# Optimization experiments

Hardware: AMD Instinct MI355X
Metric: run time of the kernel (lower is better)

Reference implementation:

```python
import jax, jax.numpy as jnp
import numpy as np
from jax import lax

HID = 256
FLAT = 32 * 9 * 9  # ShallowConv on 84x84: (84-8)/4+1=20 -> (20-4)/2+1=9 ; 32 ch


def _conv(x, w, b, stride):
    y = lax.conv_general_dilated(x, w, window_strides=(stride, stride),
                                 padding='VALID',
                                 dimension_numbers=('NCHW', 'OIHW', 'NCHW'))
    return y + b[None, :, None, None]


def setup_inputs() -> dict:
    key = jax.random.key(0)
    ks = jax.random.split(key, 20)
    seq, batch, c, h, w = 80, 128, 4, 84, 84
    n_out = 18
    f32 = jnp.float32
    inp = {}
    inp['obs'] = jax.random.uniform(ks[0], (seq, batch, c, h, w), dtype=f32)
    inp['mask'] = (jax.random.uniform(ks[1], (seq, batch)) > 0.05).astype(f32)
    inp['lstm_h'] = jax.random.normal(ks[2], (1, batch, HID), dtype=f32)
    inp['lstm_c'] = jax.random.normal(ks[3], (1, batch, HID), dtype=f32)
    inp['behaviour_actions'] = jax.random.randint(ks[4], (seq, batch), 0, n_out)
    def init(k, shape, fan_in):
        return (jax.random.normal(k, shape, dtype=f32) / np.sqrt(fan_in)).astype(f32)
    inp['conv1_w'] = init(ks[5], (16, c, 8, 8), c * 64)
    inp['conv1_b'] = jnp.zeros((16,), f32)
    inp['conv2_w'] = init(ks[6], (32, 16, 4, 4), 16 * 16)
    inp['conv2_b'] = jnp.zeros((32,), f32)
    inp['fc_w'] = init(ks[7], (HID, FLAT), FLAT)
    inp['fc_b'] = jnp.zeros((HID,), f32)
    inp['w_ih'] = init(ks[8], (4 * HID, HID), HID)
    inp['w_hh'] = init(ks[9], (4 * HID, HID), HID)
    inp['b_ih'] = jnp.zeros((4 * HID,), f32)
    inp['b_hh'] = jnp.zeros((4 * HID,), f32)
    inp['value_w'] = init(ks[10], (1, HID), HID)
    inp['value_b'] = jnp.zeros((1,), f32)
    inp['logits_w'] = init(ks[11], (n_out, HID), HID)
    inp['logits_b'] = jnp.zeros((n_out,), f32)
    return inp


def reference(obs, mask, lstm_h, lstm_c, behaviour_actions,
              conv1_w, conv1_b, conv2_w, conv2_b, fc_w, fc_b,
              w_ih, w_hh, b_ih, b_hh, value_w, value_b, logits_w, logits_b):
    seq, batch, c, h, w = obs.shape
    x = obs.reshape(seq * batch, c, h, w)
    # body: ShallowConv -> Flatten -> ReLU -> fc -> ReLU
    x = jax.nn.relu(_conv(x, conv1_w, conv1_b, 4))
    x = jax.nn.relu(_conv(x, conv2_w, conv2_b, 2))
    x = x.reshape(seq * batch, FLAT)
    x = jax.nn.relu(x @ fc_w.T + fc_b)
    x = x.reshape(seq, batch, HID)

    def step(carry, xs_t):
        hprev, cprev = carry
        xt, mt = xs_t
        gates = xt @ w_ih.T + b_ih + hprev @ w_hh.T + b_hh  # (batch, 4H)
        i, f, g, o = jnp.split(gates, 4, axis=-1)  # torch gate order i,f,g,o
        i, f, o = jax.nn.sigmoid(i), jax.nn.sigmoid(f), jax.nn.sigmoid(o)
        cn = f * cprev + i * jnp.tanh(g)
        hn = o * jnp.tanh(cn)
        m = mt[:, None]
        return (hn * m, cn * m), hn  # emit pre-mask output, mask states

    (hf, cf), hs = lax.scan(step, (lstm_h[0], lstm_c[0]), (x, mask))
    flat = hs.reshape(seq * batch, HID)
    target_value = flat @ value_w.T + value_b  # (S*B, 1)
    logits = flat @ logits_w.T + logits_b      # (S*B, n_out)
    logp = jax.nn.log_softmax(logits, axis=-1)
    acts = behaviour_actions.reshape(seq * batch)
    target_log_probs = jnp.take_along_axis(logp, acts[:, None], axis=1)
    target_entropy = -jnp.sum(jnp.exp(logp) * logp, axis=-1, keepdims=True)
    return (target_log_probs.reshape(seq, batch, 1),
            target_entropy.reshape(seq, batch, 1),
            target_value.reshape(seq, batch, 1))
```

## Files before the change

### kernel.cpp

```cpp
#include <hip/hip_runtime.h>

typedef unsigned short u16;
typedef unsigned int   u32;
typedef unsigned long long u64;
typedef short    s8v  __attribute__((ext_vector_type(8)));
typedef float    f4v  __attribute__((ext_vector_type(4)));
typedef u64      ul2v __attribute__((ext_vector_type(2)));
typedef _Float16 h2v  __attribute__((ext_vector_type(2)));

#define DEV __device__ __forceinline__

DEV u16 f2bf(float f) {
  u32 u = __builtin_bit_cast(u32, f);
  return (u16)((u + 0x8000u) >> 16);
}
DEV float bf2f(u16 b) { u32 u = ((u32)b) << 16; return __builtin_bit_cast(float, u); }
DEV void splitbf(float f, u16& hi, u16& lo) {
  hi = f2bf(f);
  lo = f2bf(f - bf2f(hi));
}
DEV u16 f2h(float f) {
  _Float16 h = (_Float16)f;
  return __builtin_bit_cast(u16, h);
}
DEV float h2f(u16 b) { _Float16 h = __builtin_bit_cast(_Float16, b); return (float)h; }
DEV float fdot2u(u32 a, u32 b, float c) {
#if __has_builtin(__builtin_amdgcn_fdot2)
  return __builtin_amdgcn_fdot2(__builtin_bit_cast(h2v, a),
                                __builtin_bit_cast(h2v, b), c, false);
#else
  h2v x = __builtin_bit_cast(h2v, a), y = __builtin_bit_cast(h2v, b);
  return c + (float)x[0]*(float)y[0] + (float)x[1]*(float)y[1];
#endif
}
DEV float sigm(float x) { return 1.f / (1.f + __expf(-x)); }
DEV f4v mfma16(s8v a, s8v b, f4v c) {
  return __builtin_amdgcn_mfma_f32_16x16x32_bf16(a, b, c, 0, 0, 0);
}
DEV u32 permpack(u32 a, u32 b) {
#if __has_builtin(__builtin_amdgcn_perm)
  return __builtin_amdgcn_perm(a, b, 0x07060302u);
#else
  return (b >> 16) | (a & 0xffff0000u);
#endif
}
DEV void split8(const float* __restrict__ ap, s8v& Ah, s8v& Al) {
  const float4 v0 = *(const float4*)ap;
  const float4 v1 = *(const float4*)(ap + 4);
  const float f[8] = {v0.x, v0.y, v0.z, v0.w, v1.x, v1.y, v1.z, v1.w};
  uint4 hh, ll;
  u32 hp[4], lp[4];
  #pragma unroll
  for (int i = 0; i < 4; ++i) {
    const u32 ua = __builtin_bit_cast(u32, f[2 * i]);
    const u32 ub = __builtin_bit_cast(u32, f[2 * i + 1]);
    const u32 ta = ua + 0x8000u, tb = ub + 0x8000u;
    hp[i] = permpack(tb, ta);
    const float la = f[2 * i]     - __builtin_bit_cast(float, ta & 0xffff0000u);
    const float lb = f[2 * i + 1] - __builtin_bit_cast(float, tb & 0xffff0000u);
    lp[i] = permpack(__builtin_bit_cast(u32, lb) + 0x8000u,
                     __builtin_bit_cast(u32, la) + 0x8000u);
  }
  hh.x = hp[0]; hh.y = hp[1]; hh.z = hp[2]; hh.w = hp[3];
  ll.x = lp[0]; ll.y = lp[1]; ll.z = lp[2]; ll.w = lp[3];
  Ah = __builtin_bit_cast(s8v, hh);
  Al = __builtin_bit_cast(s8v, ll);
}

__global__ void prep_k(const float* __restrict__ w1, const float* __restrict__ w2,
                       const float* __restrict__ fcw, const float* __restrict__ wih,
                       const float* __restrict__ whh, const float* __restrict__ bih,
                       const float* __restrict__ bhh,
                       u16* __restrict__ w1h, u16* __restrict__ w1l,
                       u16* __restrict__ w2h, u16* __restrict__ w2l,
                       u16* __restrict__ fh,  u16* __restrict__ fl,
                       u16* __restrict__ ih,  u16* __restrict__ il,
                       u16* __restrict__ whhh, float* __restrict__ bsum) {
  const int i0 = blockIdx.x * 256 + threadIdx.x;
  const int st = gridDim.x * 256;
  for (int i = i0; i < 663552; i += st) splitbf(fcw[i], fh[i], fl[i]);
  for (int i = i0; i < 262144; i += st) splitbf(wih[i], ih[i], il[i]);
  for (int i = i0; i < 262144; i += st) whhh[i] = f2h(whh[i]);
  for (int i = i0; i < 4096;   i += st) splitbf(w1[i], w1h[i], w1l[i]);
  for (int i = i0; i < 8192;   i += st) {
    const int oc = i >> 8, k = i & 255;
    const int ky = k >> 6, kx = (k >> 4) & 3, cc = k & 15;
    splitbf(w2[((oc * 16 + cc) * 4 + ky) * 4 + kx], w2h[i], w2l[i]);
  }
  for (int i = i0; i < 1024; i += st) bsum[i] = bih[i] + bhh[i];
}

__global__ __launch_bounds__(256) void conv_k(const float* __restrict__ obs,
    const u16* __restrict__ w1h, const u16* __restrict__ w1l, const float* __restrict__ b1,
    const u16* __restrict__ w2h, const u16* __restrict__ w2l, const float* __restrict__ b2,
    u16* __restrict__ out2h, u16* __restrict__ out2l) {
  __shared__ __align__(16) u16 t1h[6400], t1l[6400];
  const int tid = threadIdx.x, lane = tid & 63, wid = tid >> 6;
  const int l15 = lane & 15, kc = lane >> 4;
  const int n = blockIdx.x;
  s8v bw1h[8], bw1l[8];
  #pragma unroll
  for (int k0 = 0; k0 < 8; ++k0) {
    const int o1 = l15 * 256 + k0 * 32 + kc * 8;
    bw1h[k0] = *(const s8v*)(w1h + o1);
    bw1l[k0] = *(const s8v*)(w1l + o1);
  }
  const float bias1 = b1[l15];
  const float* img = obs + (u64)n * 28224;
  for (int ch = wid; ch < 25; ch += 4) {
    const int p = ch * 16 + l15;
    const int oy = p / 20, ox = p - oy * 20;
    const float* ab = img + oy * 336 + ox * 4;
    f4v ahh = {0,0,0,0}, ahl = {0,0,0,0}, alh = {0,0,0,0};
    #pragma unroll
    for (int k0 = 0; k0 < 8; ++k0) {
      const int kb = k0 * 32 + kc * 8;
      const int c = kb >> 6, ky = (kb >> 3) & 7;
      s8v Ah, Al;
      split8(ab + c * 7056 + ky * 84, Ah, Al);
      ahh = mfma16(Ah, bw1h[k0], ahh);
      ahl = mfma16(Ah, bw1l[k0], ahl);
      alh = mfma16(Al, bw1h[k0], alh);
    }
    const int pr0 = ch * 16 + kc * 4;
    #pragma unroll
    for (int r = 0; r < 4; ++r) {
      float v = fmaxf(ahh[r] + ahl[r] + alh[r] + bias1, 0.f);
      u16 hi, lo; splitbf(v, hi, lo);
      t1h[(pr0 + r) * 16 + l15] = hi;
      t1l[(pr0 + r) * 16 + l15] = lo;
    }
  }
  __syncthreads();
  const float bb2a = b2[l15], bb2b = b2[16 + l15];
  for (int u = wid; u < 12; u += 4) {
    const int ch = u >> 1, ot = u & 1;
    const int p = ch * 16 + l15;
    const int pc = p < 81 ? p : 80;
    const int oy = pc / 9, ox = pc - oy * 9;
    const int base = (oy * 40 + ox * 2) * 16;
    f4v a0 = {0,0,0,0}, a1 = {0,0,0,0}, a2 = {0,0,0,0};
    #pragma unroll
    for (int k0 = 0; k0 < 8; ++k0) {
      const int kb = k0 * 32 + kc * 8;
      const int ky = kb >> 6, kx = (kb >> 4) & 3, c0 = kb & 15;
      const int off = base + (ky * 20 + kx) * 16 + c0;
      s8v Ah = *(const s8v*)(t1h + off);
      s8v Al = *(const s8v*)(t1l + off);
      const int wo = (ot * 16 + l15) * 256 + k0 * 32 + kc * 8;
      s8v Bh = *(const s8v*)(w2h + wo);
      s8v Bl = *(const s8v*)(w2l + wo);
      a0 = mfma16(Ah, Bh, a0);
      a1 = mfma16(Ah, Bl, a1);
      a2 = mfma16(Al, Bh, a2);
    }
    const float bb = ot ? bb2b : bb2a;
    const int oc = ot * 16 + l15;
    u16* dh = out2h + (u64)n * 2592 + oc * 81;
    u16* dl = out2l + (u64)n * 2592 + oc * 81;
    const int pr0 = ch * 16 + kc * 4;
    #pragma unroll
    for (int r = 0; r < 4; ++r) {
      const int pp = pr0 + r;
      if (pp < 81) {
        float v = fmaxf(a0[r] + a1[r] + a2[r] + bb, 0.f);
        u16 hi, lo; splitbf(v, hi, lo);
        dh[pp] = hi;
        dl[pp] = lo;
      }
    }
  }
}

template <int RELU, int OSPLIT>
__global__ __launch_bounds__(256) void gemm3_k(const u16* __restrict__ Ah,
    const u16* __restrict__ Al, const u16* __restrict__ Bh, const u16* __restrict__ Bl,
    const float* __restrict__ bias, void* __restrict__ o1, void* __restrict__ o2,
    int M, int N, int K) {
  __shared__ __align__(16) u16 lAh[4096], lAl[4096];
  __shared__ __align__(16) u16 lBh[4096], lBl[4096];
  const int tid = threadIdx.x, lane = tid & 63, wid = tid >> 6;
  const int nb = N >> 7;
  const int bm = (int)blockIdx.x / nb, bn = (int)blockIdx.x % nb;
  const int m0 = bm << 7, n0 = bn << 7;
  const int wr = wid >> 1, wc = wid & 1;
  const int l15 = lane & 15, l4 = lane >> 4;
  f4v acc[4][4] = {};
  const int srow = tid >> 2;
  const int scol = (tid & 3) << 3;
  const u64 rA0 = (u64)(m0 + srow) * K + scol;
  const u64 rA1 = (u64)(m0 + 64 + srow) * K + scol;
  const u64 rB0 = (u64)(n0 + srow) * K + scol;
  const u64 rB1 = (u64)(n0 + 64 + srow) * K + scol;
  for (int k0 = 0; k0 < K; k0 += 32) {
    uint4 vah0 = *(const uint4*)(Ah + rA0 + k0);
    uint4 vah1 = *(const uint4*)(Ah + rA1 + k0);
    uint4 val0 = *(const uint4*)(Al + rA0 + k0);
    uint4 val1 = *(const uint4*)(Al + rA1 + k0);
    uint4 vbh0 = *(const uint4*)(Bh + rB0 + k0);
    uint4 vbh1 = *(const uint4*)(Bh + rB1 + k0);
    uint4 vbl0 = *(const uint4*)(Bl + rB0 + k0);
    uint4 vbl1 = *(const uint4*)(Bl + rB1 + k0);
    __syncthreads();
    ((uint4*)lAh)[tid] = vah0;  ((uint4*)lAh)[256 + tid] = vah1;
    ((uint4*)lAl)[tid] = val0;  ((uint4*)lAl)[256 + tid] = val1;
    ((uint4*)lBh)[tid] = vbh0;  ((uint4*)lBh)[256 + tid] = vbh1;
    ((uint4*)lBl)[tid] = vbl0;  ((uint4*)lBl)[256 + tid] = vbl1;
    __syncthreads();
    s8v afh[4], afl[4], bfh[4], bfl[4];
    #pragma unroll
    for (int a = 0; a < 4; ++a) {
      const int off = (wr * 64 + a * 16 + l15) * 32 + l4 * 8;
      afh[a] = *(const s8v*)(lAh + off);
      afl[a] = *(const s8v*)(lAl + off);
    }
    #pragma unroll
    for (int b = 0; b < 4; ++b) {
      const int off = (wc * 64 + b * 16 + l15) * 32 + l4 * 8;
      bfh[b] = *(const s8v*)(lBh + off);
      bfl[b] = *(const s8v*)(lBl + off);
    }
    #pragma unroll
    for (int a = 0; a < 4; ++a)
      #pragma unroll
      for (int b = 0; b < 4; ++b) {
        acc[a][b] = mfma16(afh[a], bfh[b], acc[a][b]);
        acc[a][b] = mfma16(afh[a], bfl[b], acc[a][b]);
        acc[a][b] = mfma16(afl[a], bfh[b], acc[a][b]);
      }
  }
  #pragma unroll
  for (int a = 0; a < 4; ++a) {
    const int mr = m0 + wr * 64 + a * 16 + l4 * 4;
    #pragma unroll
    for (int b = 0; b < 4; ++b) {
      const int col = n0 + wc * 64 + b * 16 + l15;
      const float bv = bias[col];
      #pragma unroll
      for (int r = 0; r < 4; ++r) {
        float v = acc[a][b][r] + bv;
        if (RELU) v = fmaxf(v, 0.f);
        const u64 idx = (u64)(mr + r) * N + col;
        if (OSPLIT) {
          u16 hi, lo; splitbf(v, hi, lo);
          ((u16*)o1)[idx] = hi;
          ((u16*)o2)[idx] = lo;
        } else {
          ((float*)o1)[idx] = v;
        }
      }
    }
  }
}

__global__ __launch_bounds__(1024) void lstm_k(const float* __restrict__ pre,
    const float* __restrict__ mask, const float* __restrict__ h0,
    const float* __restrict__ c0, const u16* __restrict__ whh,
    float* __restrict__ hs) {
  __shared__ __align__(16) uint4 lds_o[32 * 256];
  __shared__ __align__(16) float4 lds_red[3 * 256];
  __shared__ __align__(16) u32 lds_hh[128];
  __shared__ __align__(16) u32 lds_hl[128];
  const int t = threadIdx.x, b = blockIdx.x;
  const int col = t & 255, kq = t >> 8;
  uint4 wi[8], wf[8], wg[8];
  {
    const u32* wb = (const u32*)whh;
    const uint4* pi_ = (const uint4*)(wb + (u64)col * 128) + kq * 8;
    const uint4* pf_ = (const uint4*)(wb + (u64)(256 + col) * 128) + kq * 8;
    const uint4* pg_ = (const uint4*)(wb + (u64)(512 + col) * 128) + kq * 8;
    #pragma unroll
    for (int q = 0; q < 8; ++q) {
      wi[q] = pi_[q]; wf[q] = pf_[q]; wg[q] = pg_[q];
    }
    const uint4* po_ = (const uint4*)(wb + (u64)(768 + col) * 128);
    #pragma unroll
    for (int j = 0; j < 8; ++j) {
      const int kp4 = kq * 8 + j;
      lds_o[kp4 * 256 + col] = po_[kp4];
    }
  }
  float c = 0.f;
  if (kq == 0) c = c0[b * 256 + col];
  if (t < 128) {
    float a0 = h0[b * 256 + 2 * t], a1 = h0[b * 256 + 2 * t + 1];
    u16 h0a = f2h(a0); u16 l0a = f2h(a0 - h2f(h0a));
    u16 h1a = f2h(a1); u16 l1a = f2h(a1 - h2f(h1a));
    lds_hh[t] = (u32)h0a | ((u32)h1a << 16);
    lds_hl[t] = (u32)l0a | ((u32)l1a << 16);
  }
  float npi = 0.f, npf = 0.f, npg = 0.f, npo = 0.f;
  if (kq == 0) {
    const float* pr = pre + (u64)b * 1024;
    npi = pr[col]; npf = pr[256 + col]; npg = pr[512 + col]; npo = pr[768 + col];
  }
  __syncthreads();
  for (int s = 0; s < 80; ++s) {
    float ai = npi, afv = npf, ag = npg, ao = npo;
    #pragma unroll
    for (int j = 0; j < 8; ++j) {
      const int kk = kq * 8 + j;
      const uint4 ov = lds_o[kk * 256 + col];
      const uint4 hh = ((const uint4*)lds_hh)[kk];
      const uint4 hl = ((const uint4*)lds_hl)[kk];
      ai  = fdot2u(wi[j].x, hh.x, ai);  ai  = fdot2u(wi[j].y, hh.y, ai);
      ai  = fdot2u(wi[j].z, hh.z, ai);  ai  = fdot2u(wi[j].w, hh.w, ai);
      ai  = fdot2u(wi[j].x, hl.x, ai);  ai  = fdot2u(wi[j].y, hl.y, ai);
      ai  = fdot2u(wi[j].z, hl.z, ai);  ai  = fdot2u(wi[j].w, hl.w, ai);
      afv = fdot2u(wf[j].x, hh.x, afv); afv = fdot2u(wf[j].y, hh.y, afv);
      afv = fdot2u(wf[j].z, hh.z, afv); afv = fdot2u(wf[j].w, hh.w, afv);
      afv = fdot2u(wf[j].x, hl.x, afv); afv = fdot2u(wf[j].y, hl.y, afv);
      afv = fdot2u(wf[j].z, hl.z, afv); afv = fdot2u(wf[j].w, hl.w, afv);
      ag  = fdot2u(wg[j].x, hh.x, ag);  ag  = fdot2u(wg[j].y, hh.y, ag);
      ag  = fdot2u(wg[j].z, hh.z, ag);  ag  = fdot2u(wg[j].w, hh.w, ag);
      ag  = fdot2u(wg[j].x, hl.x, ag);  ag  = fdot2u(wg[j].y, hl.y, ag);
      ag  = fdot2u(wg[j].z, hl.z, ag);  ag  = fdot2u(wg[j].w, hl.w, ag);
      ao  = fdot2u(ov.x, hh.x, ao);     ao  = fdot2u(ov.y, hh.y, ao);
      ao  = fdot2u(ov.z, hh.z, ao);     ao  = fdot2u(ov.w, hh.w, ao);
      ao  = fdot2u(ov.x, hl.x, ao);     ao  = fdot2u(ov.y, hl.y, ao);
      ao  = fdot2u(ov.z, hl.z, ao);     ao  = fdot2u(ov.w, hl.w, ao);
    }
    if (kq != 0) {
      float4 r; r.x = ai; r.y = afv; r.z = ag; r.w = ao;
      lds_red[(kq - 1) * 256 + col] = r;
    } else if (s + 1 < 80) {
      const float* pr = pre + (u64)((s + 1) * 128 + b) * 1024;
      npi = pr[col]; npf = pr[256 + col]; npg = pr[512 + col]; npo = pr[768 + col];
    }
    __syncthreads();
    if (kq == 0) {
      const float4 r1 = lds_red[col];
      const float4 r2 = lds_red[256 + col];
      const float4 r3 = lds_red[512 + col];
      ai += r1.x + r2.x + r3.x;
      afv += r1.y + r2.y + r3.y;
      ag += r1.z + r2.z + r3.z;
      ao += r1.w + r2.w + r3.w;
      const float m = mask[s * 128 + b];
      const float ig = sigm(ai), fg = sigm(afv), og = sigm(ao);
      const float gg = tanhf(ag);
      const float cn = fg * c + ig * gg;
      const float hn = og * tanhf(cn);
      hs[(u64)(s * 128 + b) * 256 + col] = hn;
      c = cn * m;
      const float hm = hn * m;
      u16 hhi = f2h(hm);
      u16 hlo = f2h(hm - h2f(hhi));
      ((u16*)lds_hh)[col] = hhi;
      ((u16*)lds_hl)[col] = hlo;
    }
    __syncthreads();
  }
}

__global__ __launch_bounds__(256) void heads_k(const float* __restrict__ hs,
    const float* __restrict__ vw, const float* __restrict__ vb,
    const float* __restrict__ lw, const float* __restrict__ lb,
    const int* __restrict__ acts, float* __restrict__ out) {
  const int lane = threadIdx.x & 63, wid = threadIdx.x >> 6;
  const int row = blockIdx.x * 4 + wid;
  const float4 h4 = *(const float4*)(hs + (u64)row * 256 + lane * 4);
  float lj[18];
  #pragma unroll
  for (int j = 0; j < 18; ++j) {
    const float4 w4 = *(const float4*)(lw + j * 256 + lane * 4);
    float p = h4.x * w4.x + h4.y * w4.y + h4.z * w4.z + h4.w * w4.w;
    #pragma unroll
    for (int o = 32; o > 0; o >>= 1) p += __shfl_xor(p, o, 64);
    lj[j] = p + lb[j];
  }
  const float4 v4 = *(const float4*)(vw + lane * 4);
  float val = h4.x * v4.x + h4.y * v4.y + h4.z * v4.z + h4.w * v4.w;
  #pragma unroll
  for (int o = 32; o > 0; o >>= 1) val += __shfl_xor(val, o, 64);
  val += vb[0];
  float mx = lj[0];
  #pragma unroll
  for (int j = 1; j < 18; ++j) mx = fmaxf(mx, lj[j]);
  float sum = 0.f;
  #pragma unroll
  for (int j = 0; j < 18; ++j) sum += __expf(lj[j] - mx);
  const float ls = __logf(sum);
  const int a = acts[row];
  float tlp = 0.f, ent = 0.f;
  #pragma unroll
  for (int j = 0; j < 18; ++j) {
    const float lp = lj[j] - mx - ls;
    const float pj = __expf(lp);
    ent -= pj * lp;
    if (j == a) tlp = lp;
  }
  if (lane == 0) {
    out[row]         = tlp;
    out[10240 + row] = ent;
    out[20480 + row] = val;
  }
}

extern "C" void kernel_launch(void* const* d_in, const int* in_sizes, int n_in,
                              void* d_out, int out_size, void* d_ws, size_t ws_size,
                              hipStream_t stream) {
  const float* obs  = (const float*)d_in[0];
  const float* mask = (const float*)d_in[1];
  const float* h0   = (const float*)d_in[2];
  const float* c0   = (const float*)d_in[3];
  const int*   acts = (const int*)d_in[4];
  const float* w1   = (const float*)d_in[5];
  const float* b1   = (const float*)d_in[6];
  const float* w2   = (const float*)d_in[7];
  const float* b2   = (const float*)d_in[8];
  const float* fcw  = (const float*)d_in[9];
  const float* fcb  = (const float*)d_in[10];
  const float* wih  = (const float*)d_in[11];
  const float* whh  = (const float*)d_in[12];
  const float* bih  = (const float*)d_in[13];
  const float* bhh  = (const float*)d_in[14];
  const float* vw   = (const float*)d_in[15];
  const float* vb   = (const float*)d_in[16];
  const float* lw   = (const float*)d_in[17];
  const float* lb   = (const float*)d_in[18];
  float* out = (float*)d_out;

  char* cur = (char*)d_ws;
  auto carve = [&](size_t bytes) {
    void* p = cur; cur += (bytes + 255) & ~(size_t)255; return p;
  };
  u16*   out2h = (u16*)carve(10240ULL * 2592 * 2);
  u16*   out2l = (u16*)carve(10240ULL * 2592 * 2);
  u16*   xh    = (u16*)carve(10240ULL * 256 * 2);
  u16*   xl    = (u16*)carve(10240ULL * 256 * 2);
  float* pre   = (float*)carve(10240ULL * 1024 * 4);
  float* hs    = (float*)carve(10240ULL * 256 * 4);
  u16*   w1h   = (u16*)carve(4096ULL * 2);
  u16*   w1l   = (u16*)carve(4096ULL * 2);
  u16*   w2h   = (u16*)carve(8192ULL * 2);
  u16*   w2l   = (u16*)carve(8192ULL * 2);
  u16*   fwh   = (u16*)carve(663552ULL * 2);
  u16*   fwl   = (u16*)carve(663552ULL * 2);
  u16*   iwh   = (u16*)carve(262144ULL * 2);
  u16*   iwl   = (u16*)carve(262144ULL * 2);
  u16*   whhh  = (u16*)carve(262144ULL * 2);
  float* bsum  = (float*)carve(1024ULL * 4);

  prep_k<<<512, 256, 0, stream>>>(w1, w2, fcw, wih, whh, bih, bhh,
                                  w1h, w1l, w2h, w2l, fwh, fwl, iwh, iwl, whhh, bsum);
  conv_k<<<10240, 256, 0, stream>>>(obs, w1h, w1l, b1, w2h, w2l, b2, out2h, out2l);
  gemm3_k<1, 1><<<160, 256, 0, stream>>>(out2h, out2l, fwh, fwl, fcb, xh, xl,
                                         10240, 256, 2592);
  gemm3_k<0, 0><<<640, 256, 0, stream>>>(xh, xl, iwh, iwl, bsum, pre, nullptr,
                                         10240, 1024, 256);
  lstm_k<<<128, 1024, 0, stream>>>(pre, mask, h0, c0, whhh, hs);
  heads_k<<<2560, 256, 0, stream>>>(hs, vw, vb, lw, lb, acts, out);
}
```

Baseline: 987.6 us.

## Widen conv kernel to 16 waves and store conv2 output position-major

The conv kernel now launches 1024 threads per image, so conv1 chunks spread over 16 waves and conv2 runs one wave per tile with no loop. conv1 weights are loaded from global inside the k-loop instead of being held in registers, to keep register use low enough for the larger block. conv2 output is written position-major (pos*32+oc) so the stores are coalesced, and the fc weight split in prep permutes its K dimension to match. The larger block may lower occupancy, leaves 4 waves idle during conv2, and adds repeated weight loads.

```diff
diff --git a/kernel.cpp b/kernel.cpp
--- a/kernel.cpp
+++ b/kernel.cpp
@@ -78,7 +78,11 @@
                        u16* __restrict__ whhh, float* __restrict__ bsum) {
   const int i0 = blockIdx.x * 256 + threadIdx.x;
   const int st = gridDim.x * 256;
-  for (int i = i0; i < 663552; i += st) splitbf(fcw[i], fh[i], fl[i]);
+  for (int i = i0; i < 663552; i += st) {
+    const int j = i / 2592, k2 = i - j * 2592;
+    const int pos = k2 >> 5, oc = k2 & 31;
+    splitbf(fcw[j * 2592 + oc * 81 + pos], fh[i], fl[i]);
+  }
   for (int i = i0; i < 262144; i += st) splitbf(wih[i], ih[i], il[i]);
   for (int i = i0; i < 262144; i += st) whhh[i] = f2h(whh[i]);
   for (int i = i0; i < 4096;   i += st) splitbf(w1[i], w1h[i], w1l[i]);
@@ -90,7 +94,7 @@
   for (int i = i0; i < 1024; i += st) bsum[i] = bih[i] + bhh[i];
 }
 
-__global__ __launch_bounds__(256) void conv_k(const float* __restrict__ obs,
+__global__ __launch_bounds__(1024) void conv_k(const float* __restrict__ obs,
     const u16* __restrict__ w1h, const u16* __restrict__ w1l, const float* __restrict__ b1,
     const u16* __restrict__ w2h, const u16* __restrict__ w2l, const float* __restrict__ b2,
     u16* __restrict__ out2h, u16* __restrict__ out2l) {
@@ -98,16 +102,9 @@
   const int tid = threadIdx.x, lane = tid & 63, wid = tid >> 6;
   const int l15 = lane & 15, kc = lane >> 4;
   const int n = blockIdx.x;
-  s8v bw1h[8], bw1l[8];
-  #pragma unroll
-  for (int k0 = 0; k0 < 8; ++k0) {
-    const int o1 = l15 * 256 + k0 * 32 + kc * 8;
-    bw1h[k0] = *(const s8v*)(w1h + o1);
-    bw1l[k0] = *(const s8v*)(w1l + o1);
-  }
   const float bias1 = b1[l15];
   const float* img = obs + (u64)n * 28224;
-  for (int ch = wid; ch < 25; ch += 4) {
+  for (int ch = wid; ch < 25; ch += 16) {
     const int p = ch * 16 + l15;
     const int oy = p / 20, ox = p - oy * 20;
     const float* ab = img + oy * 336 + ox * 4;
@@ -118,9 +115,12 @@
       const int c = kb >> 6, ky = (kb >> 3) & 7;
       s8v Ah, Al;
       split8(ab + c * 7056 + ky * 84, Ah, Al);
-      ahh = mfma16(Ah, bw1h[k0], ahh);
-      ahl = mfma16(Ah, bw1l[k0], ahl);
-      alh = mfma16(Al, bw1h[k0], alh);
+      const int o1 = l15 * 256 + k0 * 32 + kc * 8;
+      const s8v Bh = *(const s8v*)(w1h + o1);
+      const s8v Bl = *(const s8v*)(w1l + o1);
+      ahh = mfma16(Ah, Bh, ahh);
+      ahl = mfma16(Ah, Bl, ahl);
+      alh = mfma16(Al, Bh, alh);
     }
     const int pr0 = ch * 16 + kc * 4;
     #pragma unroll
@@ -132,9 +132,9 @@
     }
   }
   __syncthreads();
-  const float bb2a = b2[l15], bb2b = b2[16 + l15];
-  for (int u = wid; u < 12; u += 4) {
-    const int ch = u >> 1, ot = u & 1;
+  if (wid < 12) {
+    const int ch = wid >> 1, ot = wid & 1;
+    const float bb = ot ? b2[16 + l15] : b2[l15];
     const int p = ch * 16 + l15;
     const int pc = p < 81 ? p : 80;
     const int oy = pc / 9, ox = pc - oy * 9;
@@ -154,10 +154,9 @@
       a1 = mfma16(Ah, Bl, a1);
       a2 = mfma16(Al, Bh, a2);
     }
-    const float bb = ot ? bb2b : bb2a;
     const int oc = ot * 16 + l15;
-    u16* dh = out2h + (u64)n * 2592 + oc * 81;
-    u16* dl = out2l + (u64)n * 2592 + oc * 81;
+    u16* dh = out2h + (u64)n * 2592;
+    u16* dl = out2l + (u64)n * 2592;
     const int pr0 = ch * 16 + kc * 4;
     #pragma unroll
     for (int r = 0; r < 4; ++r) {
@@ -165,8 +164,8 @@
       if (pp < 81) {
         float v = fmaxf(a0[r] + a1[r] + a2[r] + bb, 0.f);
         u16 hi, lo; splitbf(v, hi, lo);
-        dh[pp] = hi;
-        dl[pp] = lo;
+        dh[pp * 32 + oc] = hi;
+        dl[pp * 32 + oc] = lo;
       }
     }
   }
@@ -444,7 +443,7 @@
 
   prep_k<<<512, 256, 0, stream>>>(w1, w2, fcw, wih, whh, bih, bhh,
                                   w1h, w1l, w2h, w2l, fwh, fwl, iwh, iwl, whhh, bsum);
-  conv_k<<<10240, 256, 0, stream>>>(obs, w1h, w1l, b1, w2h, w2l, b2, out2h, out2l);
+  conv_k<<<10240, 1024, 0, stream>>>(obs, w1h, w1l, b1, w2h, w2l, b2, out2h, out2l);
   gemm3_k<1, 1><<<160, 256, 0, stream>>>(out2h, out2l, fwh, fwl, fcb, xh, xl,
                                          10240, 256, 2592);
   gemm3_k<0, 0><<<640, 256, 0, stream>>>(xh, xl, iwh, iwl, bsum, pre, nullptr,
```

After: 1.317 ms. 1.33x slower.

## Batch conv1 loads, hoist conv2 weights, store conv2 output position-major

Applied to the files above, without the earlier changes.

Conv1 now issues all eight pairs of float4 observation loads before doing the bf16 splits and MFMAs, so more memory requests are in flight at once. Conv2 loads its weight fragments into registers before the K loop. Conv2 output is written position-major ([pos][oc]), making adjacent lanes store adjacent halves, and the fc weight prep permutes columns to match that layout. The launch bound asks for 2 blocks per CU, which may increase register pressure given the larger register arrays.

```diff
diff --git a/kernel.cpp b/kernel.cpp
--- a/kernel.cpp
+++ b/kernel.cpp
@@ -44,9 +44,7 @@
   return (b >> 16) | (a & 0xffff0000u);
 #endif
 }
-DEV void split8(const float* __restrict__ ap, s8v& Ah, s8v& Al) {
-  const float4 v0 = *(const float4*)ap;
-  const float4 v1 = *(const float4*)(ap + 4);
+DEV void split8r(float4 v0, float4 v1, s8v& Ah, s8v& Al) {
   const float f[8] = {v0.x, v0.y, v0.z, v0.w, v1.x, v1.y, v1.z, v1.w};
   uint4 hh, ll;
   u32 hp[4], lp[4];
@@ -78,7 +76,11 @@
                        u16* __restrict__ whhh, float* __restrict__ bsum) {
   const int i0 = blockIdx.x * 256 + threadIdx.x;
   const int st = gridDim.x * 256;
-  for (int i = i0; i < 663552; i += st) splitbf(fcw[i], fh[i], fl[i]);
+  for (int i = i0; i < 663552; i += st) {
+    const int j = i / 2592, k2 = i - j * 2592;
+    const int pos = k2 >> 5, oc = k2 & 31;
+    splitbf(fcw[j * 2592 + oc * 81 + pos], fh[i], fl[i]);
+  }
   for (int i = i0; i < 262144; i += st) splitbf(wih[i], ih[i], il[i]);
   for (int i = i0; i < 262144; i += st) whhh[i] = f2h(whh[i]);
   for (int i = i0; i < 4096;   i += st) splitbf(w1[i], w1h[i], w1l[i]);
@@ -90,7 +92,7 @@
   for (int i = i0; i < 1024; i += st) bsum[i] = bih[i] + bhh[i];
 }
 
-__global__ __launch_bounds__(256) void conv_k(const float* __restrict__ obs,
+__global__ __launch_bounds__(256, 2) void conv_k(const float* __restrict__ obs,
     const u16* __restrict__ w1h, const u16* __restrict__ w1l, const float* __restrict__ b1,
     const u16* __restrict__ w2h, const u16* __restrict__ w2l, const float* __restrict__ b2,
     u16* __restrict__ out2h, u16* __restrict__ out2l) {
@@ -111,13 +113,20 @@
     const int p = ch * 16 + l15;
     const int oy = p / 20, ox = p - oy * 20;
     const float* ab = img + oy * 336 + ox * 4;
-    f4v ahh = {0,0,0,0}, ahl = {0,0,0,0}, alh = {0,0,0,0};
+    float4 ra[8], rb[8];
     #pragma unroll
     for (int k0 = 0; k0 < 8; ++k0) {
       const int kb = k0 * 32 + kc * 8;
       const int c = kb >> 6, ky = (kb >> 3) & 7;
+      const float* ap = ab + c * 7056 + ky * 84;
+      ra[k0] = *(const float4*)ap;
+      rb[k0] = *(const float4*)(ap + 4);
+    }
+    f4v ahh = {0,0,0,0}, ahl = {0,0,0,0}, alh = {0,0,0,0};
+    #pragma unroll
+    for (int k0 = 0; k0 < 8; ++k0) {
       s8v Ah, Al;
-      split8(ab + c * 7056 + ky * 84, Ah, Al);
+      split8r(ra[k0], rb[k0], Ah, Al);
       ahh = mfma16(Ah, bw1h[k0], ahh);
       ahl = mfma16(Ah, bw1l[k0], ahl);
       alh = mfma16(Al, bw1h[k0], alh);
@@ -135,6 +144,13 @@
   const float bb2a = b2[l15], bb2b = b2[16 + l15];
   for (int u = wid; u < 12; u += 4) {
     const int ch = u >> 1, ot = u & 1;
+    s8v cw2h[8], cw2l[8];
+    #pragma unroll
+    for (int k0 = 0; k0 < 8; ++k0) {
+      const int wo = (ot * 16 + l15) * 256 + k0 * 32 + kc * 8;
+      cw2h[k0] = *(const s8v*)(w2h + wo);
+      cw2l[k0] = *(const s8v*)(w2l + wo);
+    }
     const int p = ch * 16 + l15;
     const int pc = p < 81 ? p : 80;
     const int oy = pc / 9, ox = pc - oy * 9;
@@ -147,17 +163,14 @@
       const int off = base + (ky * 20 + kx) * 16 + c0;
       s8v Ah = *(const s8v*)(t1h + off);
       s8v Al = *(const s8v*)(t1l + off);
-      const int wo = (ot * 16 + l15) * 256 + k0 * 32 + kc * 8;
-      s8v Bh = *(const s8v*)(w2h + wo);
-      s8v Bl = *(const s8v*)(w2l + wo);
-      a0 = mfma16(Ah, Bh, a0);
-      a1 = mfma16(Ah, Bl, a1);
-      a2 = mfma16(Al, Bh, a2);
+      a0 = mfma16(Ah, cw2h[k0], a0);
+      a1 = mfma16(Ah, cw2l[k0], a1);
+      a2 = mfma16(Al, cw2h[k0], a2);
     }
     const float bb = ot ? bb2b : bb2a;
     const int oc = ot * 16 + l15;
-    u16* dh = out2h + (u64)n * 2592 + oc * 81;
-    u16* dl = out2l + (u64)n * 2592 + oc * 81;
+    u16* dh = out2h + (u64)n * 2592;
+    u16* dl = out2l + (u64)n * 2592;
     const int pr0 = ch * 16 + kc * 4;
     #pragma unroll
     for (int r = 0; r < 4; ++r) {
@@ -165,8 +178,8 @@
       if (pp < 81) {
         float v = fmaxf(a0[r] + a1[r] + a2[r] + bb, 0.f);
         u16 hi, lo; splitbf(v, hi, lo);
-        dh[pp] = hi;
-        dl[pp] = lo;
+        dh[pp * 32 + oc] = hi;
+        dl[pp * 32 + oc] = lo;
       }
     }
   }
```

New measurement: 813.6 us, median of 2. -17.6%, faster.
